# Performance work log

Hardware: AMD Instinct MI355X
Metric: run time of the kernel (lower is better)

Reference implementation:

```python
import jax, jax.numpy as jnp
import numpy as np

B, C, H, W = 16, 256, 96, 96
CQ = C // 8      # 32, query/key channels in CrossAttention
CM = C // 2      # 128, inter_planes


def conv1x1(x, w, b=None):
    # x: [B,Cin,H,W], w: [Cout,Cin]
    y = jnp.einsum('bchw,oc->bohw', x, w)
    if b is not None:
        y = y + b[None, :, None, None]
    return y


def cross_attention(x, wq, bq, wk, bk, wv, bv, gamma):
    # criss-cross (axial H and W) attention with -inf diagonal on the H branch
    b_, c_, h_, w_ = x.shape
    q = conv1x1(x, wq, bq)  # [B,CQ,H,W]
    k = conv1x1(x, wk, bk)
    v = conv1x1(x, wv, bv)  # [B,C,H,W]
    # energy over column (H axis): [B,H,W,H], masked diag h==h'
    e_h = jnp.einsum('bchw,bckw->bhwk', q, k)
    diag = jnp.eye(h_, dtype=bool)[None, :, None, :]  # [1,H,1,H]
    e_h = jnp.where(diag, -jnp.inf, e_h)
    # energy over row (W axis): [B,H,W,W]
    e_w = jnp.einsum('bchw,bchv->bhwv', q, k)
    att = jax.nn.softmax(jnp.concatenate([e_h, e_w], axis=3), axis=3)
    a_h, a_w = att[..., :h_], att[..., h_:]
    out_h = jnp.einsum('bckw,bhwk->bchw', v, a_h)
    out_w = jnp.einsum('bchv,bhwv->bchw', v, a_w)
    return gamma * (out_h + out_w) + x


def spatial_weighted(x, w_q_right, w_v_right, w_up, b_up):
    b_, _, h_, w_ = x.shape
    inp = conv1x1(x, w_v_right).reshape(b_, CM, h_ * w_)        # [B,CM,HW]
    mask = conv1x1(x, w_q_right).reshape(b_, 1, h_ * w_)        # [B,1,HW]
    mask = jax.nn.softmax(mask, axis=2)
    ctx = jnp.einsum('bcn,bon->bco', inp, mask)                 # [B,CM,1]
    ctx = jnp.einsum('bci,oc->boi', ctx, w_up) + b_up[None, :, None]  # [B,C,1]
    mask_ch = jax.nn.sigmoid(ctx)[..., None]                    # [B,C,1,1]
    return x * mask_ch


def channel_weighted(x, w_q_left, w_v_left):
    b_, _, h_, w_ = x.shape
    g = conv1x1(x, w_q_left)                                    # [B,CM,H,W]
    avg = jnp.mean(g, axis=(2, 3))                              # [B,CM]
    theta = conv1x1(x, w_v_left).reshape(b_, CM, h_ * w_)       # [B,CM,HW]
    ctx = jnp.einsum('bc,bcn->bn', avg, theta)                  # [B,HW]
    ctx = jax.nn.softmax(ctx, axis=1).reshape(b_, 1, h_, w_)
    return x * jax.nn.sigmoid(ctx)


def setup_inputs() -> dict:
    key = jax.random.key(0)
    ks = jax.random.split(key, 16)
    s = lambda fan_in: (2.0 / fan_in) ** 0.5
    inp = {
        'x': jax.random.normal(ks[0], (B, C, H, W), jnp.float32),
        'w_q_right': jax.random.normal(ks[1], (1, C), jnp.float32) * s(C),
        'w_v_right': jax.random.normal(ks[2], (CM, C), jnp.float32) * s(C),
        'w_up': jax.random.normal(ks[3], (C, CM), jnp.float32) * s(CM),
        'b_up': jnp.zeros((C,), jnp.float32),
        'w_q_left': jax.random.normal(ks[4], (CM, C), jnp.float32) * s(C),
        'w_v_left': jax.random.normal(ks[5], (CM, C), jnp.float32) * s(C),
        'cr_wq': jax.random.normal(ks[6], (CQ, C), jnp.float32) * s(C),
        'cr_bq': jnp.zeros((CQ,), jnp.float32),
        'cr_wk': jax.random.normal(ks[7], (CQ, C), jnp.float32) * s(C),
        'cr_bk': jnp.zeros((CQ,), jnp.float32),
        'cr_wv': jax.random.normal(ks[8], (C, C), jnp.float32) * s(C),
        'cr_bv': jnp.zeros((C,), jnp.float32),
        'gamma': jax.random.normal(ks[9], (1,), jnp.float32) * 0.1,
    }
    return inp


def reference(x, w_q_right, w_v_right, w_up, b_up, w_q_left, w_v_left,
              cr_wq, cr_bq, cr_wk, cr_bk, cr_wv, cr_bv, gamma):
    cross = lambda t: cross_attention(t, cr_wq, cr_bq, cr_wk, cr_bk, cr_wv, cr_bv, gamma)
    ctx_channel = cross(spatial_weighted(x, w_q_right, w_v_right, w_up, b_up))
    ctx_spatial = cross(channel_weighted(x, w_q_left, w_v_left))
    return cross(ctx_spatial + ctx_channel)
```

## Files before the change

kernel.cpp:

```cpp
#include <hip/hip_runtime.h>
#include <math.h>

#define Bn 16
#define Cn 256
#define Hn 96
#define Wn 96
#define Nn 9216
#define PIXn 147456
#define XSZk ((size_t)Bn*Cn*Nn)
#define YSZk ((size_t)Bn*64*Nn)
#define ATTSZ ((size_t)PIXn*96)

typedef short bf8 __attribute__((ext_vector_type(8)));
typedef float f32x4 __attribute__((ext_vector_type(4)));
#define MFMA(a,b,c) __builtin_amdgcn_mfma_f32_16x16x32_bf16(a,b,c,0,0,0)

typedef unsigned short ushort_t;
typedef _Float16 h16;

__device__ inline ushort_t f2bf(float f){
  union{float f; unsigned int u;} v; v.f=f;
  unsigned int r = v.u + 0x7fffu + ((v.u>>16)&1u);
  return (ushort_t)(r>>16);
}
__device__ inline float bf2f(ushort_t s){
  union{unsigned int u; float f;} v; v.u = ((unsigned int)s)<<16;
  return v.f;
}
__device__ inline ushort_t f2h(float f){
  union{h16 h; ushort_t u;} v; v.h=(h16)f; return v.u;
}
__device__ inline float h2f(ushort_t u){
  union{ushort_t u; h16 h;} v; v.u=u; return (float)v.h;
}

__device__ inline float waveSum(float v){
#pragma unroll
  for(int o=32;o;o>>=1) v += __shfl_down(v,o,64);
  return v;
}
__device__ inline float waveMax(float v){
#pragma unroll
  for(int o=32;o;o>>=1) v = fmaxf(v,__shfl_down(v,o,64));
  return v;
}


template<int XBW>
__global__ __launch_bounds__(1024) void k_pass1(const float* __restrict__ x,
    const float* __restrict__ wqr, float* __restrict__ xmean,
    float* __restrict__ partp, ushort_t* __restrict__ XB){
  int cg = blockIdx.x, b = blockIdx.y, tid = threadIdx.x;
  __shared__ float r16[16];
  float mp[2][8];
#pragma unroll
  for(int u=0;u<2;u++)
#pragma unroll
    for(int e=0;e<8;e++) mp[u][e]=0.f;
  for(int cc=0;cc<16;cc++){
    int c = cg*16+cc;
    const float* row = x + ((size_t)b*Cn + c)*Nn;
    float w = wqr[c];
    float s = 0.f;
#pragma unroll
    for(int u=0;u<2;u++){
      int ch = tid + u*1024;
      if(ch < 1152){
        float4 a = *(const float4*)&row[ch*8];
        float4 d = *(const float4*)&row[ch*8+4];
        float v0=a.x,v1=a.y,v2=a.z,v3=a.w,v4=d.x,v5=d.y,v6=d.z,v7=d.w;
        s += ((v0+v1)+(v2+v3))+((v4+v5)+(v6+v7));
        mp[u][0]+=w*v0; mp[u][1]+=w*v1; mp[u][2]+=w*v2; mp[u][3]+=w*v3;
        mp[u][4]+=w*v4; mp[u][5]+=w*v5; mp[u][6]+=w*v6; mp[u][7]+=w*v7;
        if(XBW){
          uint4 pk;
          pk.x=(unsigned)f2bf(v0)|((unsigned)f2bf(v1)<<16);
          pk.y=(unsigned)f2bf(v2)|((unsigned)f2bf(v3)<<16);
          pk.z=(unsigned)f2bf(v4)|((unsigned)f2bf(v5)<<16);
          pk.w=(unsigned)f2bf(v6)|((unsigned)f2bf(v7)<<16);
          *(uint4*)&XB[((size_t)b*Cn + c)*Nn + ch*8] = pk;
        }
      }
    }
    s = waveSum(s);
    if((tid&63)==0) r16[tid>>6]=s;
    __syncthreads();
    if(tid==0){
      float t=0.f;
      for(int i=0;i<16;i++) t+=r16[i];
      xmean[(size_t)b*Cn + c] = t*(1.f/Nn);
    }
    __syncthreads();
  }
  float* dst = partp + ((size_t)cg*Bn + b)*Nn;
#pragma unroll
  for(int u=0;u<2;u++){
    int ch = tid + u*1024;
    if(ch < 1152){
      float4 o1, o2;
      o1.x=mp[u][0]; o1.y=mp[u][1]; o1.z=mp[u][2]; o1.w=mp[u][3];
      o2.x=mp[u][4]; o2.y=mp[u][5]; o2.z=mp[u][6]; o2.w=mp[u][7];
      *(float4*)&dst[ch*8]   = o1;
      *(float4*)&dst[ch*8+4] = o2;
    }
  }
}

template<int XBR>
__global__ __launch_bounds__(1024) void k_pass2(const float* __restrict__ x,
    const ushort_t* __restrict__ XB, const float* __restrict__ wvec,
    const float* __restrict__ maskb, float* __restrict__ xw,
    float* __restrict__ partp){
  int cg = blockIdx.x, b = blockIdx.y, tid = threadIdx.x;
  __shared__ float r16[16];
  float cp[2][8], mk[2][8];
#pragma unroll
  for(int u=0;u<2;u++){
    int ch = tid + u*1024;
    if(ch < 1152){
      float4 a = *(const float4*)&maskb[(size_t)b*Nn + ch*8];
      float4 d = *(const float4*)&maskb[(size_t)b*Nn + ch*8 + 4];
      mk[u][0]=a.x; mk[u][1]=a.y; mk[u][2]=a.z; mk[u][3]=a.w;
      mk[u][4]=d.x; mk[u][5]=d.y; mk[u][6]=d.z; mk[u][7]=d.w;
    }
#pragma unroll
    for(int e=0;e<8;e++) cp[u][e]=0.f;
  }
  for(int cc=0;cc<16;cc++){
    int c = cg*16+cc;
    float w = wvec[(size_t)b*Cn + c];
    float s = 0.f;
#pragma unroll
    for(int u=0;u<2;u++){
      int ch = tid + u*1024;
      if(ch < 1152){
        float v[8];
        if(XBR){
          uint4 q = *(const uint4*)&XB[((size_t)b*Cn + c)*Nn + ch*8];
          unsigned* qp=(unsigned*)&q;
#pragma unroll
          for(int k=0;k<4;k++){
            v[2*k]   = bf2f((ushort_t)(qp[k]&0xffff));
            v[2*k+1] = bf2f((ushort_t)(qp[k]>>16));
          }
        } else {
          const float* row = x + ((size_t)b*Cn + c)*Nn;
          float4 a = *(const float4*)&row[ch*8];
          float4 d = *(const float4*)&row[ch*8+4];
          v[0]=a.x; v[1]=a.y; v[2]=a.z; v[3]=a.w;
          v[4]=d.x; v[5]=d.y; v[6]=d.z; v[7]=d.w;
        }
#pragma unroll
        for(int e=0;e<8;e++){
          s += mk[u][e]*v[e];
          cp[u][e] += w*v[e];
        }
      }
    }
    s = waveSum(s);
    if((tid&63)==0) r16[tid>>6]=s;
    __syncthreads();
    if(tid==0){
      float t=0.f;
      for(int i=0;i<16;i++) t+=r16[i];
      xw[(size_t)b*Cn + c] = t;
    }
    __syncthreads();
  }
  float* dst = partp + ((size_t)cg*Bn + b)*Nn;
#pragma unroll
  for(int u=0;u<2;u++){
    int ch = tid + u*1024;
    if(ch < 1152){
      float4 o1, o2;
      o1.x=cp[u][0]; o1.y=cp[u][1]; o1.z=cp[u][2]; o1.w=cp[u][3];
      o2.x=cp[u][4]; o2.y=cp[u][5]; o2.z=cp[u][6]; o2.w=cp[u][7];
      *(float4*)&dst[ch*8]   = o1;
      *(float4*)&dst[ch*8+4] = o2;
    }
  }
}

__global__ void k_red16(const float* __restrict__ part, float* __restrict__ out){
  size_t p = (size_t)blockIdx.x*256 + threadIdx.x;
  float s=0.f;
#pragma unroll
  for(int cg=0;cg<16;cg++) s += part[(size_t)cg*Bn*Nn + p];
  out[p]=s;
}

__device__ inline void softmax_n_body(const float* __restrict__ in,
    float* __restrict__ out, int b, int mode){
  int tid=threadIdx.x, lane=tid&63, wid=tid>>6;
  const float* p = in + (size_t)b*Nn;
  __shared__ float red[16];
  __shared__ float bc2[2];
  float mx=-3e38f;
  for(int i=tid;i<Nn;i+=1024) mx=fmaxf(mx,p[i]);
  mx = waveMax(mx);
  if(lane==0) red[wid]=mx;
  __syncthreads();
  if(tid==0){ float m=red[0]; for(int i=1;i<16;i++) m=fmaxf(m,red[i]); bc2[0]=m; }
  __syncthreads();
  mx=bc2[0];
  float s=0.f;
  for(int i=tid;i<Nn;i+=1024) s+=expf(p[i]-mx);
  s = waveSum(s);
  __syncthreads();
  if(lane==0) red[wid]=s;
  __syncthreads();
  if(tid==0){ float t=0.f; for(int i=0;i<16;i++) t+=red[i]; bc2[1]=t; }
  __syncthreads();
  float inv=1.f/bc2[1];
  for(int i=tid;i<Nn;i+=1024){
    float e=expf(p[i]-mx)*inv;
    out[(size_t)b*Nn+i] = mode ? 1.f/(1.f+expf(-e)) : e;
  }
}

__global__ __launch_bounds__(1024) void k_sn1(const float* __restrict__ mraw,
    float* __restrict__ maskb, const float* __restrict__ xmean,
    const float* __restrict__ wql, const float* __restrict__ wvl,
    float* __restrict__ wvec){
  if(blockIdx.x < 16){
    softmax_n_body(mraw, maskb, blockIdx.x, 0);
  } else {
    int b = blockIdx.x - 16, t = threadIdx.x;
    __shared__ float xm[Cn];
    __shared__ float av[128];
    if(t<Cn) xm[t] = xmean[b*Cn+t];
    __syncthreads();
    if(t<128){
      float s=0.f;
      for(int c=0;c<Cn;c++) s += wql[t*Cn+c]*xm[c];
      av[t]=s;
    }
    __syncthreads();
    if(t<Cn){
      float s=0.f;
      for(int m=0;m<128;m++) s += av[m]*wvl[m*Cn+t];
      wvec[b*Cn+t]=s;
    }
  }
}

__global__ __launch_bounds__(1024) void k_sn2(const float* __restrict__ craw,
    float* __restrict__ m2, const float* __restrict__ xw,
    const float* __restrict__ wvr, const float* __restrict__ wup,
    const float* __restrict__ bup, float* __restrict__ g1){
  if(blockIdx.x < 16){
    softmax_n_body(craw, m2, blockIdx.x, 1);
  } else {
    int b = blockIdx.x - 16, t = threadIdx.x;
    __shared__ float xs[Cn];
    __shared__ float cx[128];
    if(t<Cn) xs[t]=xw[b*Cn+t];
    __syncthreads();
    if(t<128){
      float s=0.f;
      for(int c=0;c<Cn;c++) s += wvr[t*Cn+c]*xs[c];
      cx[t]=s;
    }
    __syncthreads();
    if(t<Cn){
      float s=bup[t];
      for(int m=0;m<128;m++) s += wup[t*128+m]*cx[m];
      g1[b*Cn+t]=1.f/(1.f+expf(-s));
    }
  }
}


__global__ void k_packb(const float* __restrict__ wq, const float* __restrict__ bq,
                        const float* __restrict__ wk, const float* __restrict__ bk,
                        const float* __restrict__ wv, const float* __restrict__ bv,
                        ushort_t* __restrict__ Wp, float* __restrict__ bp){
  int o = blockIdx.x, t = threadIdx.x;
  const float* src; float bs;
  if(o<32){ src = wq + o*Cn; bs = bq[o]; }
  else if(o<64){ src = wk + (o-32)*Cn; bs = bk[o-32]; }
  else { src = wv + (o-64)*Cn; bs = bv[o-64]; }
  Wp[o*Cn+t] = f2bf(src[t]);
  if(t==0) bp[o] = bs;
}

#define AP 40
#define BP 264
#define GP 68

template<int GATED, int XBR>
__global__ __launch_bounds__(256) void k_gemm_qkv(
    const ushort_t* __restrict__ tb, const float* __restrict__ x,
    const ushort_t* __restrict__ XBp,
    const float* __restrict__ g1, const float* __restrict__ m2,
    const ushort_t* __restrict__ Wp, const float* __restrict__ bp,
    ushort_t* __restrict__ Yqk, ushort_t* __restrict__ Vb, int sel){
  __shared__ ushort_t SM[320*AP + 64*BP];
  __shared__ float gsh[256];
  ushort_t* Ws = SM;
  ushort_t* Bt = SM + 320*AP;
  int b = blockIdx.y;
  int n0 = blockIdx.x*64;
  int tid = threadIdx.x, lane = tid&63, wid = tid>>6;

  if(GATED){
    gsh[tid] = g1[b*Cn + tid];
    __syncthreads();
    float scl_n = (sel==1) ? m2[(size_t)b*Nn + n0 + (tid&63)] : 0.f;
    int cg = (tid>>6)*8;
#pragma unroll
    for(int p=0;p<8;p++){
      int c8 = p*32 + cg;
      float fv[8];
      if(XBR){
        const ushort_t* xb = XBp + (size_t)b*Cn*Nn + n0 + (tid&63);
#pragma unroll
        for(int k2=0;k2<8;k2++){
          float xf = bf2f(xb[(size_t)(c8+k2)*Nn]);
          fv[k2] = xf * (sel==0 ? gsh[c8+k2] : scl_n);
        }
      } else {
        const float* xb = x + (size_t)b*Cn*Nn + n0 + (tid&63);
#pragma unroll
        for(int k2=0;k2<8;k2++){
          float xf = xb[(size_t)(c8+k2)*Nn];
          fv[k2] = xf * (sel==0 ? gsh[c8+k2] : scl_n);
        }
      }
      uint4 pk;
      pk.x = (unsigned)f2bf(fv[0]) | ((unsigned)f2bf(fv[1])<<16);
      pk.y = (unsigned)f2bf(fv[2]) | ((unsigned)f2bf(fv[3])<<16);
      pk.z = (unsigned)f2bf(fv[4]) | ((unsigned)f2bf(fv[5])<<16);
      pk.w = (unsigned)f2bf(fv[6]) | ((unsigned)f2bf(fv[7])<<16);
      *(uint4*)&Bt[(tid&63)*BP + c8] = pk;
    }
  } else {
    const ushort_t* xb = tb + (size_t)b*Cn*Nn + n0 + (tid&63);
    int cg = (tid>>6)*8;
#pragma unroll
    for(int p=0;p<8;p++){
      int c8 = p*32 + cg;
      unsigned e0=xb[(size_t)(c8+0)*Nn], e1=xb[(size_t)(c8+1)*Nn];
      unsigned e2=xb[(size_t)(c8+2)*Nn], e3=xb[(size_t)(c8+3)*Nn];
      unsigned e4=xb[(size_t)(c8+4)*Nn], e5=xb[(size_t)(c8+5)*Nn];
      unsigned e6=xb[(size_t)(c8+6)*Nn], e7=xb[(size_t)(c8+7)*Nn];
      uint4 pk;
      pk.x = e0 | (e1<<16); pk.y = e2 | (e3<<16);
      pk.z = e4 | (e5<<16); pk.w = e6 | (e7<<16);
      *(uint4*)&Bt[(tid&63)*BP + c8] = pk;
    }
  }

  f32x4 acc[5][4];
#pragma unroll
  for(int f=0;f<5;f++)
#pragma unroll
    for(int g=0;g<4;g++) acc[f][g] = (f32x4){0.f,0.f,0.f,0.f};

  for(int ki=0;ki<8;ki++){
    __syncthreads();
#pragma unroll
    for(int q=0;q<5;q++){
      int fidx = q*256 + tid;
      int o = fidx>>2, kk = (fidx&3)*8;
      uint4 wv = *(const uint4*)&Wp[o*Cn + ki*32 + kk];
      *(uint4*)&Ws[o*AP + kk] = wv;
    }
    __syncthreads();
    bf8 bfr[4];
#pragma unroll
    for(int g=0;g<4;g++)
      bfr[g] = *(const bf8*)&Bt[(g*16 + (lane&15))*BP + ki*32 + (lane>>4)*8];
#pragma unroll
    for(int f=0;f<5;f++){
      bf8 a = *(const bf8*)&Ws[(wid*80 + f*16 + (lane&15))*AP + (lane>>4)*8];
#pragma unroll
      for(int g=0;g<4;g++) acc[f][g] = MFMA(a, bfr[g], acc[f][g]);
    }
  }

  __syncthreads();
#pragma unroll
  for(int f=0;f<5;f++){
    int o = wid*80 + f*16 + (lane>>4)*4;
#pragma unroll
    for(int i=0;i<4;i++){
      float bias = bp[o+i];
#pragma unroll
      for(int g=0;g<4;g++)
        SM[(o+i)*GP + g*16 + (lane&15)] = f2bf(acc[f][g][i] + bias);
    }
  }
  __syncthreads();
  for(int u=tid; u<320*8; u+=256){
    int lo_ = u>>3, c8 = (u&7)*8;
    ushort_t* dst = (lo_<64) ? (Yqk + ((size_t)b*64 + lo_)*Nn)
                             : (Vb + ((size_t)b*Cn + (lo_-64))*Nn);
    *(uint4*)&dst[n0 + c8] = *(uint4*)&SM[lo_*GP + c8];
  }
}

__global__ __launch_bounds__(256) void k_transpose_b(const ushort_t* __restrict__ src,
                                                     ushort_t* __restrict__ dst){
  __shared__ ushort_t Ls[96*98];
  size_t base = (size_t)blockIdx.x * Nn;
  int tid = threadIdx.x;
  for(int e=tid*2; e<Nn; e+=512){
    unsigned int u = *(const unsigned int*)&src[base+e];
    int r=e/96, c=e%96;
    *(unsigned int*)&Ls[r*98+c] = u;
  }
  __syncthreads();
  for(int e=tid*2; e<Nn; e+=512){
    int r=e/96, c=e%96;
    unsigned int u = (unsigned int)Ls[c*98+r] | (((unsigned int)Ls[(c+1)*98+r])<<16);
    *(unsigned int*)&dst[base+e] = u;
  }
}

__global__ __launch_bounds__(256) void k_e2(const ushort_t* __restrict__ Yqk,
    const ushort_t* __restrict__ Yqkt, ushort_t* __restrict__ attl,
    ushort_t* __restrict__ attr){
  __shared__ ushort_t Qt[96*AP];
  __shared__ ushort_t Kt[96*AP];
  int r = blockIdx.x, mode = blockIdx.y, b = blockIdx.z;
  const ushort_t* Y = mode ? Yqk : Yqkt;
  int pm   = mode ? 1  : 96;
  int pr   = mode ? 96 : 1;
  ushort_t* attx = mode ? attr : attl;
  int tid = threadIdx.x, lane = tid&63, wid = tid>>6;
  {
    int half = tid>>7;
    int cg   = (tid>>5)&3;
    int l32  = tid&31;
    ushort_t* T = half ? Kt : Qt;
    const ushort_t* S = Y + ((size_t)b*64 + half*32 + cg*8)*Nn + (size_t)r*96;
#pragma unroll
    for(int p=0;p<3;p++){
      int sp = p*32 + l32;
      unsigned e0=S[(size_t)0*Nn+sp], e1=S[(size_t)1*Nn+sp];
      unsigned e2=S[(size_t)2*Nn+sp], e3=S[(size_t)3*Nn+sp];
      unsigned e4=S[(size_t)4*Nn+sp], e5=S[(size_t)5*Nn+sp];
      unsigned e6=S[(size_t)6*Nn+sp], e7=S[(size_t)7*Nn+sp];
      uint4 pk;
      pk.x = e0 | (e1<<16); pk.y = e2 | (e3<<16);
      pk.z = e4 | (e5<<16); pk.w = e6 | (e7<<16);
      *(uint4*)&T[sp*AP + cg*8] = pk;
    }
  }
  __syncthreads();
  int mb = (wid>>1)*48, nb = (wid&1)*48;
  const f32x4 z4 = {0.f,0.f,0.f,0.f};
  f32x4 acc[3][3];
  bf8 a[3], bb[3];
#pragma unroll
  for(int f=0;f<3;f++) a[f] = *(const bf8*)&Qt[(mb+f*16+(lane&15))*AP + (lane>>4)*8];
#pragma unroll
  for(int g=0;g<3;g++) bb[g] = *(const bf8*)&Kt[(nb+g*16+(lane&15))*AP + (lane>>4)*8];
#pragma unroll
  for(int f=0;f<3;f++)
#pragma unroll
    for(int g=0;g<3;g++) acc[f][g] = MFMA(a[f], bb[g], z4);
#pragma unroll
  for(int f=0;f<3;f++)
#pragma unroll
    for(int i=0;i<4;i++){
      int m = mb + f*16 + (lane>>4)*4 + i;
      ushort_t* arow = attx + ((size_t)b*Nn + (size_t)m*pm + (size_t)r*pr)*96;
#pragma unroll
      for(int g=0;g<3;g++){
        int n = nb + g*16 + (lane&15);
        arow[n] = f2h(acc[f][g][i]);
      }
    }
}

__global__ __launch_bounds__(256) void k_smvt(ushort_t* attl, ushort_t* attr,
    const ushort_t* __restrict__ Vsrc, ushort_t* __restrict__ Vdst){
  __shared__ ushort_t Ls[96*98];
  int b = blockIdx.z;
  if(blockIdx.x < 1164){
    int wave = threadIdx.x>>6, l = threadIdx.x&63;
    int t = blockIdx.x*4 + wave;
    int i=0, base=0;
    while(base + (96-i) <= t){ base += 96-i; i++; }
    int j = i + (t-base);
    int hf = l>>5, l32 = l&31;
    int h = hf ? j : i, w = hf ? i : j;
    size_t p = (size_t)b*Nn + (size_t)h*96 + w;
    const ushort_t* al = attl + p*96;
    const ushort_t* ar = attr + p*96;
    float v[6];
#pragma unroll
    for(int k=0;k<3;k++){
      int el = l32 + 32*k;
      float vv = h2f(al[el]);
      v[k] = (el==h) ? -1e30f : vv;
    }
#pragma unroll
    for(int k=0;k<3;k++) v[3+k] = h2f(ar[l32 + 32*k]);
    float mx = v[0];
#pragma unroll
    for(int k=1;k<6;k++) mx = fmaxf(mx, v[k]);
#pragma unroll
    for(int o=16;o;o>>=1) mx = fmaxf(mx, __shfl_xor(mx, o, 64));
    float e[6], s=0.f;
#pragma unroll
    for(int k=0;k<6;k++){ e[k]=expf(v[k]-mx); s+=e[k]; }
#pragma unroll
    for(int o=16;o;o>>=1) s += __shfl_xor(s, o, 64);
    float inv = 1.f/s;
    size_t q = (size_t)b*Nn + (size_t)w*96 + h;
    ushort_t* oh = attl + q*96;
    ushort_t* ow = attr + p*96;
#pragma unroll
    for(int k=0;k<3;k++) oh[l32+32*k] = f2bf(e[k]*inv);
#pragma unroll
    for(int k=0;k<3;k++) ow[l32+32*k] = f2bf(e[3+k]*inv);
  } else {
    int c = blockIdx.x - 1164;
    size_t base = ((size_t)b*Cn + c) * Nn;
    int tid = threadIdx.x;
    for(int e=tid*2; e<Nn; e+=512){
      unsigned int u = *(const unsigned int*)&Vsrc[base+e];
      int r=e/96, cc=e%96;
      *(unsigned int*)&Ls[r*98+cc] = u;
    }
    __syncthreads();
    for(int e=tid*2; e<Nn; e+=512){
      int r=e/96, cc=e%96;
      unsigned int u = (unsigned int)Ls[cc*98+r] | (((unsigned int)Ls[(cc+1)*98+r])<<16);
      *(unsigned int*)&Vdst[base+e] = u;
    }
  }
}

#define SP 104
#define RP 100

template<int RES, int XBR>
__global__ __launch_bounds__(256) void k_pv2(const ushort_t* __restrict__ VB,
    const ushort_t* __restrict__ VTb, const ushort_t* __restrict__ attw,
    const ushort_t* __restrict__ atth, const float* __restrict__ x,
    const ushort_t* __restrict__ XBp,
    const float* __restrict__ g1, const float* __restrict__ m2,
    const ushort_t* __restrict__ residb, ushort_t* __restrict__ Tob,
    ushort_t* __restrict__ OTb, const float* __restrict__ gp, int sel){
  __shared__ ushort_t SMEM[96*SP];
  int r = blockIdx.x, mode = blockIdx.y>>1, half = blockIdx.y&1, b = blockIdx.z;
  float gm = gp[0];
  int tid = threadIdx.x, lane = tid&63, wid = tid>>6;
  const ushort_t* V = mode ? VTb : VB;
  size_t vbase = (size_t)b*Cn*Nn + (size_t)r*96;
  bf8 vf[6];
#pragma unroll
  for(int f=0;f<2;f++)
#pragma unroll
    for(int j=0;j<3;j++)
      vf[f*3+j] = *(const bf8*)&V[vbase
        + (size_t)(half*128 + wid*32 + f*16 + (lane&15))*Nn + j*32 + (lane>>4)*8];
  const ushort_t* ab = (mode ? atth : attw) + ((size_t)b*Nn + (size_t)r*96)*96;
  for(int u=tid; u<96*12; u+=256){
    int n=u/12, j8=(u%12)*8;
    uint4 q = *(const uint4*)&ab[n*96 + j8];
    *(uint4*)&SMEM[n*SP + j8] = q;
  }
  __syncthreads();
  f32x4 acc[2][6];
#pragma unroll
  for(int f=0;f<2;f++)
#pragma unroll
    for(int g=0;g<6;g++) acc[f][g] = (f32x4){0.f,0.f,0.f,0.f};
#pragma unroll
  for(int j0=0;j0<3;j0++){
    bf8 bfr[6];
#pragma unroll
    for(int g=0;g<6;g++)
      bfr[g] = *(const bf8*)&SMEM[(g*16+(lane&15))*SP + j0*32 + (lane>>4)*8];
#pragma unroll
    for(int f=0;f<2;f++)
#pragma unroll
      for(int g=0;g<6;g++) acc[f][g] = MFMA(vf[f*3+j0], bfr[g], acc[f][g]);
  }
#pragma unroll
  for(int ph=0; ph<2; ph++){
    __syncthreads();
    {
      int f = ph;
      int rl = wid*16 + (lane>>4)*4;
#pragma unroll
      for(int i=0;i<4;i++)
#pragma unroll
        for(int g=0;g<6;g++)
          SMEM[(rl+i)*RP + g*16 + (lane&15)] = f2bf(gm*acc[f][g][i]);
    }
    __syncthreads();
    for(int u=tid; u<64*12; u+=256){
      int rl = u/12, q8 = (u%12)*8;
      int c = half*128 + (rl>>4)*32 + ph*16 + (rl&15);
      size_t row = vbase + (size_t)c*Nn;
      uint4 v = *(uint4*)&SMEM[rl*RP + q8];
      if(mode){
        *(uint4*)&OTb[row + q8] = v;
      } else {
        unsigned* vp=(unsigned*)&v;
        float rs[8];
        if(RES==1){
          uint4 rv = *(const uint4*)&residb[row + q8];
          unsigned* rp=(unsigned*)&rv;
#pragma unroll
          for(int k=0;k<4;k++){
            rs[2*k]   = bf2f((ushort_t)(rp[k]&0xffff));
            rs[2*k+1] = bf2f((ushort_t)(rp[k]>>16));
          }
        } else {
          float xv[8];
          if(XBR){
            uint4 xq = *(const uint4*)&XBp[row + q8];
            unsigned* xp=(unsigned*)&xq;
#pragma unroll
            for(int k=0;k<4;k++){
              xv[2*k]   = bf2f((ushort_t)(xp[k]&0xffff));
              xv[2*k+1] = bf2f((ushort_t)(xp[k]>>16));
            }
          } else {
            float4 x1 = *(const float4*)&x[row + q8];
            float4 x2 = *(const float4*)&x[row + q8 + 4];
            xv[0]=x1.x; xv[1]=x1.y; xv[2]=x1.z; xv[3]=x1.w;
            xv[4]=x2.x; xv[5]=x2.y; xv[6]=x2.z; xv[7]=x2.w;
          }
          if(sel==0){
            float g = g1[b*Cn + c];
#pragma unroll
            for(int k=0;k<8;k++) rs[k] = xv[k]*g;
          } else {
            float4 m1 = *(const float4*)&m2[(size_t)b*Nn + (size_t)r*96 + q8];
            float4 m2v= *(const float4*)&m2[(size_t)b*Nn + (size_t)r*96 + q8 + 4];
            float mv[8] = {m1.x,m1.y,m1.z,m1.w,m2v.x,m2v.y,m2v.z,m2v.w};
#pragma unroll
            for(int k=0;k<8;k++) rs[k] = xv[k]*mv[k];
          }
        }
        uint4 o; unsigned* op=(unsigned*)&o;
#pragma unroll
        for(int k=0;k<4;k++){
          float lo = bf2f((ushort_t)(vp[k]&0xffff)) + rs[2*k];
          float hi = bf2f((ushort_t)(vp[k]>>16))    + rs[2*k+1];
          op[k] = (unsigned)f2bf(lo) | ((unsigned)f2bf(hi)<<16);
        }
        *(uint4*)&Tob[row + q8] = o;
      }
    }
  }
}

template<int VAR>
__global__ __launch_bounds__(256) void k_merge(float* __restrict__ outf,
    ushort_t* __restrict__ outb, const ushort_t* __restrict__ add,
    const ushort_t* __restrict__ OT){
  __shared__ ushort_t Ls[96*98];
  size_t base = (size_t)blockIdx.x * Nn;
  int tid = threadIdx.x;
  for(int e=tid*2; e<Nn; e+=512){
    int r=e/96, c=e%96;
    *(unsigned int*)&Ls[r*98+c] = *(const unsigned int*)&OT[base+e];
  }
  __syncthreads();
  for(int e=tid*4; e<Nn; e+=1024){
    int r=e/96, c=e%96;
    float t0 = bf2f(Ls[(c+0)*98+r]), t1 = bf2f(Ls[(c+1)*98+r]);
    float t2 = bf2f(Ls[(c+2)*98+r]), t3 = bf2f(Ls[(c+3)*98+r]);
    if(VAR==4){
      uint2 v = *(const uint2*)&add[base+e];
      float4 o;
      o.x = bf2f((ushort_t)(v.x&0xffff)) + t0;
      o.y = bf2f((ushort_t)(v.x>>16))    + t1;
      o.z = bf2f((ushort_t)(v.y&0xffff)) + t2;
      o.w = bf2f((ushort_t)(v.y>>16))    + t3;
      *(float4*)&outf[base+e] = o;
    } else {
      uint2 u = *(uint2*)&outb[base+e];
      float a0 = bf2f((ushort_t)(u.x&0xffff)) + t0;
      float a1 = bf2f((ushort_t)(u.x>>16))    + t1;
      float a2 = bf2f((ushort_t)(u.y&0xffff)) + t2;
      float a3 = bf2f((ushort_t)(u.y>>16))    + t3;
      if(VAR==2){
        uint2 v = *(const uint2*)&add[base+e];
        a0 += bf2f((ushort_t)(v.x&0xffff));
        a1 += bf2f((ushort_t)(v.x>>16));
        a2 += bf2f((ushort_t)(v.y&0xffff));
        a3 += bf2f((ushort_t)(v.y>>16));
      }
      u.x = (unsigned)f2bf(a0) | ((unsigned)f2bf(a1)<<16);
      u.y = (unsigned)f2bf(a2) | ((unsigned)f2bf(a3)<<16);
      *(uint2*)&outb[base+e] = u;
    }
  }
}

extern "C" void kernel_launch(void* const* d_in, const int* in_sizes, int n_in,
                              void* d_out, int out_size, void* d_ws, size_t ws_size,
                              hipStream_t stream){
  const float* x    = (const float*)d_in[0];
  const float* wqr  = (const float*)d_in[1];
  const float* wvr  = (const float*)d_in[2];
  const float* wup  = (const float*)d_in[3];
  const float* bup  = (const float*)d_in[4];
  const float* wql  = (const float*)d_in[5];
  const float* wvl  = (const float*)d_in[6];
  const float* crwq = (const float*)d_in[7];
  const float* crbq = (const float*)d_in[8];
  const float* crwk = (const float*)d_in[9];
  const float* crbk = (const float*)d_in[10];
  const float* crwv = (const float*)d_in[11];
  const float* crbv = (const float*)d_in[12];
  const float* gma  = (const float*)d_in[13];
  float* out = (float*)d_out;

  char* wsb = (char*)d_ws;
  ushort_t* TT   = (ushort_t*)wsb; wsb += 2*XSZk*2;
  ushort_t* VB2  = (ushort_t*)wsb; wsb += XSZk*2;
  ushort_t* VT2  = (ushort_t*)wsb; wsb += XSZk*2;
  ushort_t* Y2   = (ushort_t*)wsb; wsb += YSZk*2;
  ushort_t* Yt2  = (ushort_t*)wsb; wsb += YSZk*2;
  ushort_t* ATTL = (ushort_t*)wsb; wsb += ATTSZ*2;
  ushort_t* ATTR = (ushort_t*)wsb; wsb += ATTSZ*2;
  float*    partp= (float*)wsb;    wsb += (size_t)16*Bn*Nn*4;
  ushort_t* Wpb  = (ushort_t*)wsb; wsb += 320*Cn*2;
  float*    bp   = (float*)wsb;    wsb += 320*4;
  float*    xmean= (float*)wsb;    wsb += Bn*Cn*4;
  float*    wvec = (float*)wsb;    wsb += Bn*Cn*4;
  float*    xw   = (float*)wsb;    wsb += Bn*Cn*4;
  float*    g1   = (float*)wsb;    wsb += Bn*Cn*4;
  float*    mraw = (float*)wsb;    wsb += (size_t)PIXn*4;
  float*    maskb= (float*)wsb;    wsb += (size_t)PIXn*4;
  float*    craw = (float*)wsb;    wsb += (size_t)PIXn*4;
  float*    m2   = (float*)wsb;    wsb += (size_t)PIXn*4;
  ushort_t* XB   = (ushort_t*)wsb;
  const int useXB = (ws_size >= (size_t)484000000) ? 1 : 0;

  k_packb<<<320,256,0,stream>>>(crwq,crbq,crwk,crbk,crwv,crbv,Wpb,bp);

  if(useXB) k_pass1<1><<<dim3(16,Bn),1024,0,stream>>>(x, wqr, xmean, partp, XB);
  else      k_pass1<0><<<dim3(16,Bn),1024,0,stream>>>(x, wqr, xmean, partp, nullptr);
  k_red16<<<Bn*Nn/256,256,0,stream>>>(partp, mraw);
  k_sn1<<<32,1024,0,stream>>>(mraw, maskb, xmean, wql, wvl, wvec);
  if(useXB) k_pass2<1><<<dim3(16,Bn),1024,0,stream>>>(nullptr, XB, wvec, maskb, xw, partp);
  else      k_pass2<0><<<dim3(16,Bn),1024,0,stream>>>(x, nullptr, wvec, maskb, xw, partp);
  k_red16<<<Bn*Nn/256,256,0,stream>>>(partp, craw);
  k_sn2<<<32,1024,0,stream>>>(craw, m2, xw, wvr, wup, bup, g1);

  ushort_t* T2p = TT + XSZk;

  auto crossg = [&](int sel){
    if(useXB) k_gemm_qkv<1,1><<<dim3(Nn/64,Bn),256,0,stream>>>(nullptr, nullptr, XB, g1, m2, Wpb, bp, Y2, VB2, sel);
    else      k_gemm_qkv<1,0><<<dim3(Nn/64,Bn),256,0,stream>>>(nullptr, x, nullptr, g1, m2, Wpb, bp, Y2, VB2, sel);
    k_transpose_b<<<Bn*64,256,0,stream>>>(Y2, Yt2);
    k_e2<<<dim3(96,2,Bn),256,0,stream>>>(Y2, Yt2, ATTL, ATTR);
    k_smvt<<<dim3(1164+256,1,Bn),256,0,stream>>>(ATTL, ATTR, VB2, VT2);
    ushort_t* To = TT + (size_t)sel*XSZk;
    if(useXB) k_pv2<0,1><<<dim3(96,4,Bn),256,0,stream>>>(VB2, VT2, ATTR, ATTL, nullptr, XB, g1, m2, nullptr, To, VT2, gma, sel);
    else      k_pv2<0,0><<<dim3(96,4,Bn),256,0,stream>>>(VB2, VT2, ATTR, ATTL, x, nullptr, g1, m2, nullptr, To, VT2, gma, sel);
  };

  crossg(0);
  k_merge<0><<<Bn*Cn,256,0,stream>>>(nullptr, TT, nullptr, VT2);
  crossg(1);
  k_merge<2><<<Bn*Cn,256,0,stream>>>(nullptr, TT, T2p, VT2);

  k_gemm_qkv<0,0><<<dim3(Nn/64,Bn),256,0,stream>>>(TT, nullptr, nullptr, nullptr, nullptr, Wpb, bp, Y2, VB2, 0);
  k_transpose_b<<<Bn*64,256,0,stream>>>(Y2, Yt2);
  k_e2<<<dim3(96,2,Bn),256,0,stream>>>(Y2, Yt2, ATTL, ATTR);
  k_smvt<<<dim3(1164+256,1,Bn),256,0,stream>>>(ATTL, ATTR, VB2, VT2);
  k_pv2<1,0><<<dim3(96,4,Bn),256,0,stream>>>(VB2, VT2, ATTR, ATTL,
      nullptr, nullptr, nullptr, nullptr, TT, T2p, VT2, gma, 0);
  k_merge<4><<<Bn*Cn,256,0,stream>>>(out, nullptr, T2p, VT2);
}
```

Baseline: 1.064 ms.

## Fuse criss-cross softmax into PV kernel and merge V transpose with Y transpose

Removes the standalone softmax kernel, which read raw fp16 energies and wrote normalized bf16 attention back to global memory. The PV kernel now computes the softmax while it stages each row's attention into shared memory. The V transpose moves into the Y transpose launch, so one kernel launch per cross-attention pass goes away. In exchange, each softmax row is recomputed redundantly in the 4 PV blocks (2 modes times 2 channel halves) that need it. Those blocks also do scalar strided reads of both energy tensors instead of vectorized loads of precomputed attention.

Measured after the change: 1.197 ms. 12.4% more time.

```diff
diff --git a/kernel.cpp b/kernel.cpp
--- a/kernel.cpp
+++ b/kernel.cpp
@@ -400,13 +400,18 @@
   }
 }
 
-__global__ __launch_bounds__(256) void k_transpose_b(const ushort_t* __restrict__ src,
-                                                     ushort_t* __restrict__ dst){
+__global__ __launch_bounds__(256) void k_tr2(const ushort_t* __restrict__ Ysrc,
+    ushort_t* __restrict__ Ydst, const ushort_t* __restrict__ Vsrc,
+    ushort_t* __restrict__ Vdst){
   __shared__ ushort_t Ls[96*98];
-  size_t base = (size_t)blockIdx.x * Nn;
+  int idx = blockIdx.x;
+  const int nY = Bn*64;
+  const ushort_t* src; ushort_t* dst;
+  if(idx < nY){ src = Ysrc + (size_t)idx*Nn; dst = Ydst + (size_t)idx*Nn; }
+  else { src = Vsrc + (size_t)(idx-nY)*Nn; dst = Vdst + (size_t)(idx-nY)*Nn; }
   int tid = threadIdx.x;
   for(int e=tid*2; e<Nn; e+=512){
-    unsigned int u = *(const unsigned int*)&src[base+e];
+    unsigned int u = *(const unsigned int*)&src[e];
     int r=e/96, c=e%96;
     *(unsigned int*)&Ls[r*98+c] = u;
   }
@@ -414,7 +419,7 @@
   for(int e=tid*2; e<Nn; e+=512){
     int r=e/96, c=e%96;
     unsigned int u = (unsigned int)Ls[c*98+r] | (((unsigned int)Ls[(c+1)*98+r])<<16);
-    *(unsigned int*)&dst[base+e] = u;
+    *(unsigned int*)&dst[e] = u;
   }
 }
 
@@ -475,73 +480,13 @@
     }
 }
 
-__global__ __launch_bounds__(256) void k_smvt(ushort_t* attl, ushort_t* attr,
-    const ushort_t* __restrict__ Vsrc, ushort_t* __restrict__ Vdst){
-  __shared__ ushort_t Ls[96*98];
-  int b = blockIdx.z;
-  if(blockIdx.x < 1164){
-    int wave = threadIdx.x>>6, l = threadIdx.x&63;
-    int t = blockIdx.x*4 + wave;
-    int i=0, base=0;
-    while(base + (96-i) <= t){ base += 96-i; i++; }
-    int j = i + (t-base);
-    int hf = l>>5, l32 = l&31;
-    int h = hf ? j : i, w = hf ? i : j;
-    size_t p = (size_t)b*Nn + (size_t)h*96 + w;
-    const ushort_t* al = attl + p*96;
-    const ushort_t* ar = attr + p*96;
-    float v[6];
-#pragma unroll
-    for(int k=0;k<3;k++){
-      int el = l32 + 32*k;
-      float vv = h2f(al[el]);
-      v[k] = (el==h) ? -1e30f : vv;
-    }
-#pragma unroll
-    for(int k=0;k<3;k++) v[3+k] = h2f(ar[l32 + 32*k]);
-    float mx = v[0];
-#pragma unroll
-    for(int k=1;k<6;k++) mx = fmaxf(mx, v[k]);
-#pragma unroll
-    for(int o=16;o;o>>=1) mx = fmaxf(mx, __shfl_xor(mx, o, 64));
-    float e[6], s=0.f;
-#pragma unroll
-    for(int k=0;k<6;k++){ e[k]=expf(v[k]-mx); s+=e[k]; }
-#pragma unroll
-    for(int o=16;o;o>>=1) s += __shfl_xor(s, o, 64);
-    float inv = 1.f/s;
-    size_t q = (size_t)b*Nn + (size_t)w*96 + h;
-    ushort_t* oh = attl + q*96;
-    ushort_t* ow = attr + p*96;
-#pragma unroll
-    for(int k=0;k<3;k++) oh[l32+32*k] = f2bf(e[k]*inv);
-#pragma unroll
-    for(int k=0;k<3;k++) ow[l32+32*k] = f2bf(e[3+k]*inv);
-  } else {
-    int c = blockIdx.x - 1164;
-    size_t base = ((size_t)b*Cn + c) * Nn;
-    int tid = threadIdx.x;
-    for(int e=tid*2; e<Nn; e+=512){
-      unsigned int u = *(const unsigned int*)&Vsrc[base+e];
-      int r=e/96, cc=e%96;
-      *(unsigned int*)&Ls[r*98+cc] = u;
-    }
-    __syncthreads();
-    for(int e=tid*2; e<Nn; e+=512){
-      int r=e/96, cc=e%96;
-      unsigned int u = (unsigned int)Ls[cc*98+r] | (((unsigned int)Ls[(cc+1)*98+r])<<16);
-      *(unsigned int*)&Vdst[base+e] = u;
-    }
-  }
-}
-
 #define SP 104
 #define RP 100
 
 template<int RES, int XBR>
 __global__ __launch_bounds__(256) void k_pv2(const ushort_t* __restrict__ VB,
-    const ushort_t* __restrict__ VTb, const ushort_t* __restrict__ attw,
-    const ushort_t* __restrict__ atth, const float* __restrict__ x,
+    const ushort_t* __restrict__ VTb, const ushort_t* __restrict__ attl,
+    const ushort_t* __restrict__ attr, const float* __restrict__ x,
     const ushort_t* __restrict__ XBp,
     const float* __restrict__ g1, const float* __restrict__ m2,
     const ushort_t* __restrict__ residb, ushort_t* __restrict__ Tob,
@@ -559,11 +504,40 @@
     for(int j=0;j<3;j++)
       vf[f*3+j] = *(const bf8*)&V[vbase
         + (size_t)(half*128 + wid*32 + f*16 + (lane&15))*Nn + j*32 + (lane>>4)*8];
-  const ushort_t* ab = (mode ? atth : attw) + ((size_t)b*Nn + (size_t)r*96)*96;
-  for(int u=tid; u<96*12; u+=256){
-    int n=u/12, j8=(u%12)*8;
-    uint4 q = *(const uint4*)&ab[n*96 + j8];
-    *(uint4*)&SMEM[n*SP + j8] = q;
+  {
+    int hw = tid>>5, l32 = tid&31;
+#pragma unroll
+    for(int pass=0; pass<12; pass++){
+      int n = pass*8 + hw;
+      size_t p = (size_t)b*Nn + (mode ? (size_t)n*96 + r : (size_t)r*96 + n);
+      int mel = mode ? n : r;
+      const ushort_t* al = attl + p*96;
+      const ushort_t* ar = attr + p*96;
+      float vl[3], vr[3];
+#pragma unroll
+      for(int k=0;k<3;k++){
+        int el = l32 + 32*k;
+        float t = h2f(al[el]);
+        vl[k] = (el==mel) ? -1e30f : t;
+        vr[k] = h2f(ar[el]);
+      }
+      float mx = fmaxf(fmaxf(fmaxf(vl[0],vl[1]),fmaxf(vl[2],vr[0])),fmaxf(vr[1],vr[2]));
+#pragma unroll
+      for(int o=16;o;o>>=1) mx = fmaxf(mx, __shfl_xor(mx, o, 32));
+      float s = 0.f;
+      float e[6];
+      e[0]=expf(vl[0]-mx); e[1]=expf(vl[1]-mx); e[2]=expf(vl[2]-mx);
+      e[3]=expf(vr[0]-mx); e[4]=expf(vr[1]-mx); e[5]=expf(vr[2]-mx);
+      s = ((e[0]+e[1])+(e[2]+e[3]))+(e[4]+e[5]);
+#pragma unroll
+      for(int o=16;o;o>>=1) s += __shfl_xor(s, o, 32);
+      float inv = 1.f/s;
+#pragma unroll
+      for(int k=0;k<3;k++){
+        float val = (mode ? e[k] : e[3+k]) * inv;
+        SMEM[n*SP + l32 + 32*k] = f2bf(val);
+      }
+    }
   }
   __syncthreads();
   f32x4 acc[2][6];
@@ -755,12 +729,11 @@
   auto crossg = [&](int sel){
     if(useXB) k_gemm_qkv<1,1><<<dim3(Nn/64,Bn),256,0,stream>>>(nullptr, nullptr, XB, g1, m2, Wpb, bp, Y2, VB2, sel);
     else      k_gemm_qkv<1,0><<<dim3(Nn/64,Bn),256,0,stream>>>(nullptr, x, nullptr, g1, m2, Wpb, bp, Y2, VB2, sel);
-    k_transpose_b<<<Bn*64,256,0,stream>>>(Y2, Yt2);
+    k_tr2<<<Bn*64 + Bn*Cn,256,0,stream>>>(Y2, Yt2, VB2, VT2);
     k_e2<<<dim3(96,2,Bn),256,0,stream>>>(Y2, Yt2, ATTL, ATTR);
-    k_smvt<<<dim3(1164+256,1,Bn),256,0,stream>>>(ATTL, ATTR, VB2, VT2);
     ushort_t* To = TT + (size_t)sel*XSZk;
-    if(useXB) k_pv2<0,1><<<dim3(96,4,Bn),256,0,stream>>>(VB2, VT2, ATTR, ATTL, nullptr, XB, g1, m2, nullptr, To, VT2, gma, sel);
-    else      k_pv2<0,0><<<dim3(96,4,Bn),256,0,stream>>>(VB2, VT2, ATTR, ATTL, x, nullptr, g1, m2, nullptr, To, VT2, gma, sel);
+    if(useXB) k_pv2<0,1><<<dim3(96,4,Bn),256,0,stream>>>(VB2, VT2, ATTL, ATTR, nullptr, XB, g1, m2, nullptr, To, VT2, gma, sel);
+    else      k_pv2<0,0><<<dim3(96,4,Bn),256,0,stream>>>(VB2, VT2, ATTL, ATTR, x, nullptr, g1, m2, nullptr, To, VT2, gma, sel);
   };
 
   crossg(0);
@@ -769,10 +742,9 @@
   k_merge<2><<<Bn*Cn,256,0,stream>>>(nullptr, TT, T2p, VT2);
 
   k_gemm_qkv<0,0><<<dim3(Nn/64,Bn),256,0,stream>>>(TT, nullptr, nullptr, nullptr, nullptr, Wpb, bp, Y2, VB2, 0);
-  k_transpose_b<<<Bn*64,256,0,stream>>>(Y2, Yt2);
+  k_tr2<<<Bn*64 + Bn*Cn,256,0,stream>>>(Y2, Yt2, VB2, VT2);
   k_e2<<<dim3(96,2,Bn),256,0,stream>>>(Y2, Yt2, ATTL, ATTR);
-  k_smvt<<<dim3(1164+256,1,Bn),256,0,stream>>>(ATTL, ATTR, VB2, VT2);
-  k_pv2<1,0><<<dim3(96,4,Bn),256,0,stream>>>(VB2, VT2, ATTR, ATTL,
+  k_pv2<1,0><<<dim3(96,4,Bn),256,0,stream>>>(VB2, VT2, ATTL, ATTR,
       nullptr, nullptr, nullptr, nullptr, TT, T2p, VT2, gma, 0);
   k_merge<4><<<Bn*Cn,256,0,stream>>>(out, nullptr, T2p, VT2);
 }
```
